# Kernel tuning notes

Measured on AMD Instinct MI355X. Metric: run time of the kernel, lower is better.

Reference implementation:

```python
import math
import jax, jax.numpy as jnp
import numpy as np

B, D, H = 8, 2048, 256

def setup_inputs() -> dict:
    key = jax.random.key(0)
    ks = jax.random.split(key, 8)
    s = 1.0 / math.sqrt(H)
    x = jax.random.normal(ks[0], (B, D, H), dtype=jnp.float32)
    adj = jax.random.randint(ks[1], (B, D, D), 0, 2, dtype=jnp.int32)
    Wq = jax.random.normal(ks[2], (H, H), dtype=jnp.float32) * s
    Wk = jax.random.normal(ks[3], (H, H), dtype=jnp.float32) * s
    Wv = jax.random.normal(ks[4], (H, H), dtype=jnp.float32) * s
    Wp = jax.random.normal(ks[5], (H, H), dtype=jnp.float32) * s
    bp = jax.random.normal(ks[6], (H,), dtype=jnp.float32) * 0.01
    gamma = jnp.ones((H,), dtype=jnp.float32)
    beta = jnp.zeros((H,), dtype=jnp.float32)
    return {"x": x, "adj": adj, "Wq": Wq, "Wk": Wk, "Wv": Wv,
            "Wp": Wp, "bp": bp, "gamma": gamma, "beta": beta}

def _layer_norm(h, gamma, beta, eps=1e-5):
    mu = jnp.mean(h, axis=-1, keepdims=True)
    var = jnp.mean(jnp.square(h - mu), axis=-1, keepdims=True)
    return (h - mu) * jax.lax.rsqrt(var + eps) * gamma + beta

def reference(x, adj, Wq, Wk, Wv, Wp, bp, gamma, beta):
    # torch Linear: y = x @ W.T
    q = jnp.einsum('bdh,oh->bdo', x, Wq)
    k = jnp.einsum('bdh,oh->bdo', x, Wk)
    v = jnp.einsum('bdh,oh->bdo', x, Wv)
    scores = jnp.einsum('bdo,beo->bde', q, k) / math.sqrt(H)
    scores = jnp.where(adj <= 0, jnp.float32(-1e9), scores)
    attn = jax.nn.softmax(scores, axis=-1)
    agg = jnp.einsum('bde,beo->bdo', attn, v)
    out = jnp.einsum('bdo,po->bdp', agg, Wp) + bp
    return _layer_norm(x + out, gamma, beta)
```

## Files before the change

kernel.cpp:

```cpp
#include <hip/hip_runtime.h>
#include <stdint.h>

#define NB 8
#define ND 2048
#define NH 256

typedef __attribute__((ext_vector_type(8))) short bf16x8;
typedef __attribute__((ext_vector_type(4))) float f32x4;
typedef __attribute__((ext_vector_type(16))) float f32x16;
typedef __attribute__((ext_vector_type(4))) int   i32x4;
typedef __attribute__((ext_vector_type(2))) unsigned int u32x2;
typedef __attribute__((ext_vector_type(4))) unsigned int u32x4;

#define MFMA16 __builtin_amdgcn_mfma_f32_16x16x32_bf16
#define MFMA32 __builtin_amdgcn_mfma_f32_32x32x16_bf16

__device__ __forceinline__ unsigned short f2bf(float f) {
    union { float f; unsigned int u; } c; c.f = f;
    unsigned int u = c.u + 0x7FFFu + ((c.u >> 16) & 1u);
    return (unsigned short)(u >> 16);
}
__device__ __forceinline__ unsigned int pack2(float a, float b) {
    return (unsigned int)f2bf(a) | ((unsigned int)f2bf(b) << 16);
}
__device__ __forceinline__ unsigned int cvtpk(float a, float b) {
    unsigned int r;
    asm("v_cvt_pk_bf16_f32 %0, %1, %2" : "=v"(r) : "v"(a), "v"(b));
    return r;
}
__device__ __forceinline__ void plswap(unsigned int& a, unsigned int& b) {
    asm volatile("v_permlane32_swap_b32 %0, %1" : "+v"(a), "+v"(b));
}
__device__ __forceinline__ bf16x8 mk8(unsigned int a, unsigned int b, unsigned int c, unsigned int d) {
    union { unsigned int u[4]; bf16x8 v; } x;
    x.u[0] = a; x.u[1] = b; x.u[2] = c; x.u[3] = d;
    return x.v;
}
__device__ __forceinline__ void gload_lds16(const void* g, void* l) {
    __builtin_amdgcn_global_load_lds(
        (const __attribute__((address_space(1))) void*)g,
        (__attribute__((address_space(3))) void*)l, 16, 0, 0);
}

__global__ __launch_bounds__(256) void qkv_kernel(
    const float* __restrict__ x,
    const float* __restrict__ Wq, const float* __restrict__ Wk, const float* __restrict__ Wv,
    unsigned short* __restrict__ qb, unsigned short* __restrict__ kb, unsigned short* __restrict__ vT)
{
    __shared__ unsigned short Wt[64][264];
    __shared__ unsigned short Xt[64][264];
    const int z  = blockIdx.z;
    const int m0 = blockIdx.x * 64;
    const int o0 = blockIdx.y * 64;
    const float* W = (z == 0) ? Wq : (z == 1 ? Wk : Wv);
    const int t = threadIdx.x;

#pragma unroll
    for (int i = 0; i < 16; ++i) {
        int fidx = i * 256 + t;
        int row = fidx >> 6, c4 = fidx & 63;
        f32x4 vW = *reinterpret_cast<const f32x4*>(W + (size_t)(o0 + row) * NH + c4 * 4);
        f32x4 vX = *reinterpret_cast<const f32x4*>(x + (size_t)(m0 + row) * NH + c4 * 4);
        u32x2 pw; pw[0] = pack2(vW[0], vW[1]); pw[1] = pack2(vW[2], vW[3]);
        u32x2 px; px[0] = pack2(vX[0], vX[1]); px[1] = pack2(vX[2], vX[3]);
        *reinterpret_cast<u32x2*>(&Wt[row][c4 * 4]) = pw;
        *reinterpret_cast<u32x2*>(&Xt[row][c4 * 4]) = px;
    }
    __syncthreads();

    const int w = t >> 6, lane = t & 63, lr = lane & 15, half = lane >> 4;
    const unsigned short (*Ab)[264] = (z == 2) ? Xt : Wt;
    const unsigned short (*Bb)[264] = (z == 2) ? Wt : Xt;
    const int ar0 = 32 * (w >> 1), br0 = 32 * (w & 1);

    f32x4 acc[2][2] = {};
#pragma unroll
    for (int kk = 0; kk < 8; ++kk) {
        bf16x8 a[2], bfr[2];
#pragma unroll
        for (int f = 0; f < 2; ++f) {
            a[f]   = *reinterpret_cast<const bf16x8*>(&Ab[ar0 + 16 * f + lr][32 * kk + 8 * half]);
            bfr[f] = *reinterpret_cast<const bf16x8*>(&Bb[br0 + 16 * f + lr][32 * kk + 8 * half]);
        }
#pragma unroll
        for (int fa = 0; fa < 2; ++fa)
#pragma unroll
            for (int fb = 0; fb < 2; ++fb)
                acc[fa][fb] = MFMA16(a[fa], bfr[fb], acc[fa][fb], 0, 0, 0);
    }

    if (z == 0) {
#pragma unroll
        for (int fa = 0; fa < 2; ++fa)
#pragma unroll
            for (int fb = 0; fb < 2; ++fb) {
                int m = m0 + br0 + 16 * fb + lr;
                int o = o0 + ar0 + 16 * fa + 4 * half;
                u32x2 pk; pk[0] = pack2(acc[fa][fb][0], acc[fa][fb][1]);
                pk[1] = pack2(acc[fa][fb][2], acc[fa][fb][3]);
                *reinterpret_cast<u32x2*>(qb + (size_t)m * NH + o) = pk;
            }
    } else if (z == 1) {
#pragma unroll
        for (int fa = 0; fa < 2; ++fa)
#pragma unroll
            for (int fb = 0; fb < 2; ++fb) {
                int m = m0 + br0 + 16 * fb + lr;
                int o = o0 + ar0 + 16 * fa + 4 * half;
                int bb = m >> 11, el = m & 2047;
                u32x2 pk; pk[0] = pack2(acc[fa][fb][0], acc[fa][fb][1]);
                pk[1] = pack2(acc[fa][fb][2], acc[fa][fb][3]);
                size_t idx = (((size_t)bb * 32 + (o >> 3)) * 2048 + el) * 8 + (o & 7);
                *reinterpret_cast<u32x2*>(kb + idx) = pk;
            }
    } else {
#pragma unroll
        for (int fa = 0; fa < 2; ++fa)
#pragma unroll
            for (int fb = 0; fb < 2; ++fb) {
                int dg = m0 + ar0 + 16 * fa + 4 * half;
                int o  = o0 + br0 + 16 * fb + lr;
                int bb = dg >> 11, el = dg & 2047;
                u32x2 pk; pk[0] = pack2(acc[fa][fb][0], acc[fa][fb][1]);
                pk[1] = pack2(acc[fa][fb][2], acc[fa][fb][3]);
                size_t idx = (((size_t)bb * 256 + (el >> 3)) * 256 + o) * 8 + (el & 7);
                *reinterpret_cast<u32x2*>(vT + idx) = pk;
            }
    }
}

template<int ESP, int SIDES>
__global__ __launch_bounds__(512, 2) void attn_kernel(
    const unsigned short* __restrict__ qb, const unsigned short* __restrict__ kb,
    const unsigned short* __restrict__ vT, const int* __restrict__ adj,
    unsigned short* __restrict__ part, float* __restrict__ mpart, float* __restrict__ lpart)
{
    constexpr int GROUPS = 8 / SIDES;
    constexpr int QB = 32 * GROUPS;
    constexpr int NOT = 8 / SIDES;
    constexpr int NT = (ND / ESP) / 32;
    constexpr int QTSH = (ESP == 4) ? 5 : 4;

    __shared__ unsigned char KT[2][16384];
    __shared__ unsigned char VTl[2][16384];

    const int bid = blockIdx.x;
    const int b = bid & 7, es = (bid >> 3) & (ESP - 1), qt = bid >> QTSH;
    const int t = threadIdx.x, w = t >> 6, l = t & 63;
    const int lo32 = l & 31, hi = l >> 5;
    const int g = w & (GROUPS - 1), side = w / GROUPS;
    const int qbase = qt * QB + g * 32;
    const int obase = side * (256 / SIDES);
    const int ebase = es * (ND / ESP);
    const float SC = 0.0625f, L2E = 1.44269504f;

    bf16x8 qf[16];
    {
        const unsigned short* qr = qb + ((size_t)b * ND + qbase + lo32) * NH + 8 * hi;
#pragma unroll
        for (int kk = 0; kk < 16; ++kk)
            qf[kk] = *reinterpret_cast<const bf16x8*>(qr + kk * 16);
    }

    const char* kbc = (const char*)kb + ((size_t)b << 20);
    const char* vtc = (const char*)vT + ((size_t)b << 20);
    const int* adjr = adj + ((size_t)b * ND + qbase + lo32) * ND + ebase;

    auto stageK = [&](int buf, int tt) {
        const int e0s = ebase + tt * 32;
#pragma unroll
        for (int i = 0; i < 2; ++i) {
            int off = i * 8192 + t * 16;
            int koct = off >> 9, e = (off >> 4) & 31;
            gload_lds16(kbc + (size_t)koct * 32768 + (size_t)(e0s + e) * 16, &KT[buf][off]);
        }
    };
    auto stageV = [&](int buf, int tt) {
        const int Eb = (ebase + tt * 32) >> 3;
#pragma unroll
        for (int i = 0; i < 2; ++i) {
            int off = i * 8192 + t * 16;
            int eoct = off >> 12, o = (off >> 4) & 255;
            gload_lds16(vtc + (size_t)(Eb + eoct) * 4096 + (size_t)o * 16, &VTl[buf][off]);
        }
    };

    f32x16 acc[NOT] = {};
    float m_run = -__builtin_inff(), l_run = 0.f;

    stageK(0, 0); stageV(0, 0);
    __syncthreads();

    for (int tt = 0; tt < NT; ++tt) {
        const int cur = tt & 1;
        if (tt < NT - 1) { stageK(cur ^ 1, tt + 1); stageV(cur ^ 1, tt + 1); }

        i32x4 aj[4];
#pragma unroll
        for (int gg = 0; gg < 4; ++gg)
            aj[gg] = *reinterpret_cast<const i32x4*>(adjr + tt * 32 + gg * 8 + 4 * hi);

        const char* Kc = (const char*)&KT[cur][0];
        f32x16 s = {};
#pragma unroll
        for (int kk = 0; kk < 16; ++kk) {
            bf16x8 kf = *reinterpret_cast<const bf16x8*>(Kc + kk * 1024 + hi * 512 + lo32 * 16);
            s = MFMA32(kf, qf[kk], s, 0, 0, 0);
        }

        float p[16];
        float tmax = -__builtin_inff();
#pragma unroll
        for (int gg = 0; gg < 4; ++gg)
#pragma unroll
            for (int r = 0; r < 4; ++r) {
                float sv = s[gg * 4 + r] * SC;
                sv = (aj[gg][r] > 0) ? sv : -1e9f;
                p[gg * 4 + r] = sv;
                tmax = fmaxf(tmax, sv);
            }
        tmax = fmaxf(tmax, __shfl_xor(tmax, 32));
        if (!__all(tmax <= m_run + 8.0f)) {
            const float m_new = fmaxf(m_run, tmax);
            const float scale = exp2f((m_run - m_new) * L2E);
#pragma unroll
            for (int ot = 0; ot < NOT; ++ot)
#pragma unroll
                for (int r = 0; r < 16; ++r) acc[ot][r] *= scale;
            l_run *= scale;
            m_run = m_new;
        }
        float psum = 0.f;
#pragma unroll
        for (int r2 = 0; r2 < 16; ++r2) {
            float pe = exp2f((p[r2] - m_run) * L2E);
            p[r2] = pe;
            psum += pe;
        }
        psum += __shfl_xor(psum, 32);
        l_run += psum;

        unsigned int c0 = cvtpk(p[0], p[1]),   c1 = cvtpk(p[2], p[3]);
        unsigned int c2 = cvtpk(p[4], p[5]),   c3 = cvtpk(p[6], p[7]);
        plswap(c0, c2); plswap(c1, c3);
        unsigned int c4 = cvtpk(p[8], p[9]),   c5 = cvtpk(p[10], p[11]);
        unsigned int c6 = cvtpk(p[12], p[13]), c7 = cvtpk(p[14], p[15]);
        plswap(c4, c6); plswap(c5, c7);
        const bf16x8 pf0 = mk8(c0, c1, c2, c3);
        const bf16x8 pf1 = mk8(c4, c5, c6, c7);

        const char* Vc = (const char*)&VTl[cur][0];
#pragma unroll
        for (int ot = 0; ot < NOT; ++ot) {
            bf16x8 vf = *reinterpret_cast<const bf16x8*>(
                Vc + hi * 4096 + (size_t)(obase + ot * 32 + lo32) * 16);
            acc[ot] = MFMA32(vf, pf0, acc[ot], 0, 0, 0);
        }
#pragma unroll
        for (int ot = 0; ot < NOT; ++ot) {
            bf16x8 vf = *reinterpret_cast<const bf16x8*>(
                Vc + 8192 + hi * 4096 + (size_t)(obase + ot * 32 + lo32) * 16);
            acc[ot] = MFMA32(vf, pf1, acc[ot], 0, 0, 0);
        }
        __syncthreads();
    }

    const int qg = b * ND + qbase + lo32;
    unsigned short* pb = part + ((size_t)es * 16384 + qg) * 256;
#pragma unroll
    for (int ot = 0; ot < NOT; ++ot)
#pragma unroll
        for (int g2 = 0; g2 < 4; ++g2) {
            u32x2 pk;
            pk[0] = pack2(acc[ot][g2 * 4 + 0], acc[ot][g2 * 4 + 1]);
            pk[1] = pack2(acc[ot][g2 * 4 + 2], acc[ot][g2 * 4 + 3]);
            *reinterpret_cast<u32x2*>(pb + obase + ot * 32 + g2 * 8 + 4 * hi) = pk;
        }
    if (hi == 0 && side == 0) {
        mpart[(size_t)es * 16384 + qg] = m_run;
        lpart[(size_t)es * 16384 + qg] = l_run;
    }
}

template<int ESP>
__global__ __launch_bounds__(256) void combine_kernel(
    const unsigned short* __restrict__ part, const float* __restrict__ mpart,
    const float* __restrict__ lpart, unsigned short* __restrict__ agg)
{
    const float L2E = 1.44269504f;
    const int t = threadIdx.x;
    const int row8 = t >> 5, cw = t & 31;
    const int q = blockIdx.x * 8 + row8;

    float me[ESP], le[ESP], M = -__builtin_inff();
#pragma unroll
    for (int e = 0; e < ESP; ++e) {
        me[e] = mpart[(size_t)e * 16384 + q];
        le[e] = lpart[(size_t)e * 16384 + q];
        M = fmaxf(M, me[e]);
    }
    float wsum = 0.f;
#pragma unroll
    for (int e = 0; e < ESP; ++e) { me[e] = exp2f((me[e] - M) * L2E); wsum += me[e] * le[e]; }
    const float inv = 1.f / wsum;

    float o[8] = {};
#pragma unroll
    for (int e = 0; e < ESP; ++e) {
        u32x4 v = *reinterpret_cast<const u32x4*>(part + ((size_t)e * 16384 + q) * 256 + cw * 8);
        const float ce = me[e] * inv;
#pragma unroll
        for (int j = 0; j < 4; ++j) {
            o[2 * j]     += ce * __uint_as_float(v[j] << 16);
            o[2 * j + 1] += ce * __uint_as_float(v[j] & 0xffff0000u);
        }
    }
    u32x4 pk;
#pragma unroll
    for (int j = 0; j < 4; ++j) pk[j] = pack2(o[2 * j], o[2 * j + 1]);
    *reinterpret_cast<u32x4*>(agg + (size_t)q * 256 + cw * 8) = pk;
}

__global__ __launch_bounds__(256) void oproj_kernel(
    const unsigned short* __restrict__ agg, const float* __restrict__ Wp,
    const float* __restrict__ bp, const float* __restrict__ x, float* __restrict__ h)
{
    __shared__ unsigned short Wt[64][264];
    __shared__ unsigned short Xt[64][264];
    const int m0 = blockIdx.x * 64, p0 = blockIdx.y * 64;
    const int t = threadIdx.x;

#pragma unroll
    for (int i = 0; i < 16; ++i) {
        int fidx = i * 256 + t, row = fidx >> 6, c4 = fidx & 63;
        f32x4 vW = *reinterpret_cast<const f32x4*>(Wp + (size_t)(p0 + row) * NH + c4 * 4);
        u32x2 pw; pw[0] = pack2(vW[0], vW[1]); pw[1] = pack2(vW[2], vW[3]);
        *reinterpret_cast<u32x2*>(&Wt[row][c4 * 4]) = pw;
    }
#pragma unroll
    for (int i = 0; i < 8; ++i) {
        int fidx = i * 256 + t, row = fidx >> 5, c8 = fidx & 31;
        u32x4 vA = *reinterpret_cast<const u32x4*>(agg + (size_t)(m0 + row) * NH + c8 * 8);
        *reinterpret_cast<u32x4*>(&Xt[row][c8 * 8]) = vA;
    }
    __syncthreads();

    const int w = t >> 6, lane = t & 63, lr = lane & 15, half = lane >> 4;
    const int ar0 = 32 * (w >> 1), br0 = 32 * (w & 1);

    f32x4 acc[2][2] = {};
#pragma unroll
    for (int kk = 0; kk < 8; ++kk) {
        bf16x8 a[2], bfr[2];
#pragma unroll
        for (int f = 0; f < 2; ++f) {
            a[f]   = *reinterpret_cast<const bf16x8*>(&Wt[ar0 + 16 * f + lr][32 * kk + 8 * half]);
            bfr[f] = *reinterpret_cast<const bf16x8*>(&Xt[br0 + 16 * f + lr][32 * kk + 8 * half]);
        }
#pragma unroll
        for (int fa = 0; fa < 2; ++fa)
#pragma unroll
            for (int fb = 0; fb < 2; ++fb)
                acc[fa][fb] = MFMA16(a[fa], bfr[fb], acc[fa][fb], 0, 0, 0);
    }

#pragma unroll
    for (int fa = 0; fa < 2; ++fa)
#pragma unroll
        for (int fb = 0; fb < 2; ++fb) {
            int pcol = p0 + ar0 + 16 * fa + 4 * half;
            int m = m0 + br0 + 16 * fb + lr;
            f32x4 bias = *reinterpret_cast<const f32x4*>(bp + pcol);
            f32x4 xr   = *reinterpret_cast<const f32x4*>(x + (size_t)m * NH + pcol);
            f32x4 out;
#pragma unroll
            for (int r = 0; r < 4; ++r) out[r] = acc[fa][fb][r] + bias[r] + xr[r];
            *reinterpret_cast<f32x4*>(h + (size_t)m * NH + pcol) = out;
        }
}

__global__ __launch_bounds__(256) void ln_kernel(
    const float* __restrict__ h, const float* __restrict__ gamma,
    const float* __restrict__ beta, float* __restrict__ out)
{
    const int t = threadIdx.x, w = t >> 6, lane = t & 63;
    const size_t row = (size_t)blockIdx.x * 4 + w;
    const float* hr = h + row * NH;
    f32x4 v = *reinterpret_cast<const f32x4*>(hr + lane * 4);
    float s = v[0] + v[1] + v[2] + v[3];
#pragma unroll
    for (int off = 1; off < 64; off <<= 1) s += __shfl_xor(s, off);
    const float mu = s * (1.f / 256.f);
    f32x4 dv; float q = 0.f;
#pragma unroll
    for (int r = 0; r < 4; ++r) { dv[r] = v[r] - mu; q += dv[r] * dv[r]; }
#pragma unroll
    for (int off = 1; off < 64; off <<= 1) q += __shfl_xor(q, off);
    const float rs = rsqrtf(q * (1.f / 256.f) + 1e-5f);
    f32x4 g  = *reinterpret_cast<const f32x4*>(gamma + lane * 4);
    f32x4 be = *reinterpret_cast<const f32x4*>(beta + lane * 4);
    f32x4 o;
#pragma unroll
    for (int r = 0; r < 4; ++r) o[r] = dv[r] * rs * g[r] + be[r];
    *reinterpret_cast<f32x4*>(out + row * NH + lane * 4) = o;
}

extern "C" void kernel_launch(void* const* d_in, const int* in_sizes, int n_in,
                              void* d_out, int out_size, void* d_ws, size_t ws_size,
                              hipStream_t stream)
{
    const float* x     = (const float*)d_in[0];
    const int*   adj   = (const int*)d_in[1];
    const float* Wq    = (const float*)d_in[2];
    const float* Wk    = (const float*)d_in[3];
    const float* Wv    = (const float*)d_in[4];
    const float* Wp    = (const float*)d_in[5];
    const float* bp    = (const float*)d_in[6];
    const float* gamma = (const float*)d_in[7];
    const float* beta  = (const float*)d_in[8];

    char* ws = (char*)d_ws;
    const size_t MB = 1024 * 1024;
    unsigned short* qb    = (unsigned short*)(ws);
    unsigned short* kb    = (unsigned short*)(ws + 8 * MB);
    unsigned short* vT    = (unsigned short*)(ws + 16 * MB);
    unsigned short* agg   = qb;
    unsigned short* partb = (unsigned short*)(ws + 24 * MB);
    float* h = (float*)(ws + 8 * MB);
    float* out = (float*)d_out;

    qkv_kernel<<<dim3(256, 4, 3), 256, 0, stream>>>(x, Wq, Wk, Wv, qb, kb, vT);

    const bool big = ws_size >= (size_t)57 * MB;
    if (big) {
        float* mpart = (float*)(ws + 56 * MB);
        float* lpart = (float*)(ws + 56 * MB + 256 * 1024);
        attn_kernel<4, 1><<<dim3(256), 512, 0, stream>>>(qb, kb, vT, adj, partb, mpart, lpart);
        combine_kernel<4><<<dim3(2048), 256, 0, stream>>>(partb, mpart, lpart, agg);
    } else {
        float* mpart = (float*)(ws + 40 * MB);
        float* lpart = (float*)(ws + 40 * MB + 128 * 1024);
        attn_kernel<2, 2><<<dim3(256), 512, 0, stream>>>(qb, kb, vT, adj, partb, mpart, lpart);
        combine_kernel<2><<<dim3(2048), 256, 0, stream>>>(partb, mpart, lpart, agg);
    }

    oproj_kernel<<<dim3(256, 4), 256, 0, stream>>>(agg, Wp, bp, x, h);
    ln_kernel<<<dim3(4096), 256, 0, stream>>>(h, gamma, beta, out);
}
```

Baseline: 122.5 us.

## Fuse combine, output projection and layernorm; widen attention key tiles; merge QKV blocks

The QKV projection now computes Q, K and V in one block, reusing the converted x tile and reloading only the weight tile. The attention kernel stages 64-key tiles instead of 32, processes them as two sub-steps, and raises wave priority around the MFMA sections. The split-softmax combine, output projection, bias/residual add and layernorm are merged into a single kernel that keeps rows in LDS, removing the intermediate fp32 h buffer and two launches. The trade-offs are much larger LDS per block, which may lower occupancy, and fewer, heavier blocks in the fused epilogue.

```diff
diff --git a/kernel.cpp b/kernel.cpp
--- a/kernel.cpp
+++ b/kernel.cpp
@@ -41,6 +41,8 @@
         (const __attribute__((address_space(1))) void*)g,
         (__attribute__((address_space(3))) void*)l, 16, 0, 0);
 }
+__device__ __forceinline__ float bflo(unsigned int u) { return __uint_as_float(u << 16); }
+__device__ __forceinline__ float bfhi(unsigned int u) { return __uint_as_float(u & 0xffff0000u); }
 
 __global__ __launch_bounds__(256) void qkv_kernel(
     const float* __restrict__ x,
@@ -49,17 +51,16 @@
 {
     __shared__ unsigned short Wt[64][264];
     __shared__ unsigned short Xt[64][264];
-    const int z  = blockIdx.z;
     const int m0 = blockIdx.x * 64;
     const int o0 = blockIdx.y * 64;
-    const float* W = (z == 0) ? Wq : (z == 1 ? Wk : Wv);
     const int t = threadIdx.x;
+    const int w = t >> 6, lane = t & 63, lr = lane & 15, half = lane >> 4;
+    const int ar0 = 32 * (w >> 1), br0 = 32 * (w & 1);
 
 #pragma unroll
     for (int i = 0; i < 16; ++i) {
-        int fidx = i * 256 + t;
-        int row = fidx >> 6, c4 = fidx & 63;
-        f32x4 vW = *reinterpret_cast<const f32x4*>(W + (size_t)(o0 + row) * NH + c4 * 4);
+        int fidx = i * 256 + t, row = fidx >> 6, c4 = fidx & 63;
+        f32x4 vW = *reinterpret_cast<const f32x4*>(Wq + (size_t)(o0 + row) * NH + c4 * 4);
         f32x4 vX = *reinterpret_cast<const f32x4*>(x + (size_t)(m0 + row) * NH + c4 * 4);
         u32x2 pw; pw[0] = pack2(vW[0], vW[1]); pw[1] = pack2(vW[2], vW[3]);
         u32x2 px; px[0] = pack2(vX[0], vX[1]); px[1] = pack2(vX[2], vX[3]);
@@ -68,64 +69,77 @@
     }
     __syncthreads();
 
-    const int w = t >> 6, lane = t & 63, lr = lane & 15, half = lane >> 4;
-    const unsigned short (*Ab)[264] = (z == 2) ? Xt : Wt;
-    const unsigned short (*Bb)[264] = (z == 2) ? Wt : Xt;
-    const int ar0 = 32 * (w >> 1), br0 = 32 * (w & 1);
-
-    f32x4 acc[2][2] = {};
-#pragma unroll
-    for (int kk = 0; kk < 8; ++kk) {
-        bf16x8 a[2], bfr[2];
-#pragma unroll
-        for (int f = 0; f < 2; ++f) {
-            a[f]   = *reinterpret_cast<const bf16x8*>(&Ab[ar0 + 16 * f + lr][32 * kk + 8 * half]);
-            bfr[f] = *reinterpret_cast<const bf16x8*>(&Bb[br0 + 16 * f + lr][32 * kk + 8 * half]);
-        }
-#pragma unroll
-        for (int fa = 0; fa < 2; ++fa)
-#pragma unroll
-            for (int fb = 0; fb < 2; ++fb)
-                acc[fa][fb] = MFMA16(a[fa], bfr[fb], acc[fa][fb], 0, 0, 0);
-    }
-
-    if (z == 0) {
-#pragma unroll
-        for (int fa = 0; fa < 2; ++fa)
-#pragma unroll
-            for (int fb = 0; fb < 2; ++fb) {
-                int m = m0 + br0 + 16 * fb + lr;
-                int o = o0 + ar0 + 16 * fa + 4 * half;
-                u32x2 pk; pk[0] = pack2(acc[fa][fb][0], acc[fa][fb][1]);
-                pk[1] = pack2(acc[fa][fb][2], acc[fa][fb][3]);
-                *reinterpret_cast<u32x2*>(qb + (size_t)m * NH + o) = pk;
-            }
-    } else if (z == 1) {
-#pragma unroll
-        for (int fa = 0; fa < 2; ++fa)
-#pragma unroll
-            for (int fb = 0; fb < 2; ++fb) {
-                int m = m0 + br0 + 16 * fb + lr;
-                int o = o0 + ar0 + 16 * fa + 4 * half;
-                int bb = m >> 11, el = m & 2047;
-                u32x2 pk; pk[0] = pack2(acc[fa][fb][0], acc[fa][fb][1]);
-                pk[1] = pack2(acc[fa][fb][2], acc[fa][fb][3]);
-                size_t idx = (((size_t)bb * 32 + (o >> 3)) * 2048 + el) * 8 + (o & 7);
-                *reinterpret_cast<u32x2*>(kb + idx) = pk;
-            }
-    } else {
-#pragma unroll
-        for (int fa = 0; fa < 2; ++fa)
-#pragma unroll
-            for (int fb = 0; fb < 2; ++fb) {
-                int dg = m0 + ar0 + 16 * fa + 4 * half;
-                int o  = o0 + br0 + 16 * fb + lr;
-                int bb = dg >> 11, el = dg & 2047;
-                u32x2 pk; pk[0] = pack2(acc[fa][fb][0], acc[fa][fb][1]);
-                pk[1] = pack2(acc[fa][fb][2], acc[fa][fb][3]);
-                size_t idx = (((size_t)bb * 256 + (el >> 3)) * 256 + o) * 8 + (el & 7);
-                *reinterpret_cast<u32x2*>(vT + idx) = pk;
-            }
+    for (int z = 0; z < 3; ++z) {
+        const unsigned short (*Ab)[264] = (z == 2) ? Xt : Wt;
+        const unsigned short (*Bb)[264] = (z == 2) ? Wt : Xt;
+
+        f32x4 acc[2][2] = {};
+#pragma unroll
+        for (int kk = 0; kk < 8; ++kk) {
+            bf16x8 a[2], bfr[2];
+#pragma unroll
+            for (int f = 0; f < 2; ++f) {
+                a[f]   = *reinterpret_cast<const bf16x8*>(&Ab[ar0 + 16 * f + lr][32 * kk + 8 * half]);
+                bfr[f] = *reinterpret_cast<const bf16x8*>(&Bb[br0 + 16 * f + lr][32 * kk + 8 * half]);
+            }
+#pragma unroll
+            for (int fa = 0; fa < 2; ++fa)
+#pragma unroll
+                for (int fb = 0; fb < 2; ++fb)
+                    acc[fa][fb] = MFMA16(a[fa], bfr[fb], acc[fa][fb], 0, 0, 0);
+        }
+
+        if (z == 0) {
+#pragma unroll
+            for (int fa = 0; fa < 2; ++fa)
+#pragma unroll
+                for (int fb = 0; fb < 2; ++fb) {
+                    int m = m0 + br0 + 16 * fb + lr;
+                    int o = o0 + ar0 + 16 * fa + 4 * half;
+                    u32x2 pk; pk[0] = pack2(acc[fa][fb][0], acc[fa][fb][1]);
+                    pk[1] = pack2(acc[fa][fb][2], acc[fa][fb][3]);
+                    *reinterpret_cast<u32x2*>(qb + (size_t)m * NH + o) = pk;
+                }
+        } else if (z == 1) {
+#pragma unroll
+            for (int fa = 0; fa < 2; ++fa)
+#pragma unroll
+                for (int fb = 0; fb < 2; ++fb) {
+                    int m = m0 + br0 + 16 * fb + lr;
+                    int o = o0 + ar0 + 16 * fa + 4 * half;
+                    int bb = m >> 11, el = m & 2047;
+                    u32x2 pk; pk[0] = pack2(acc[fa][fb][0], acc[fa][fb][1]);
+                    pk[1] = pack2(acc[fa][fb][2], acc[fa][fb][3]);
+                    size_t idx = (((size_t)bb * 32 + (o >> 3)) * 2048 + el) * 8 + (o & 7);
+                    *reinterpret_cast<u32x2*>(kb + idx) = pk;
+                }
+        } else {
+#pragma unroll
+            for (int fa = 0; fa < 2; ++fa)
+#pragma unroll
+                for (int fb = 0; fb < 2; ++fb) {
+                    int dg = m0 + ar0 + 16 * fa + 4 * half;
+                    int o  = o0 + br0 + 16 * fb + lr;
+                    int bb = dg >> 11, el = dg & 2047;
+                    u32x2 pk; pk[0] = pack2(acc[fa][fb][0], acc[fa][fb][1]);
+                    pk[1] = pack2(acc[fa][fb][2], acc[fa][fb][3]);
+                    size_t idx = (((size_t)bb * 256 + (el >> 3)) * 256 + o) * 8 + (el & 7);
+                    *reinterpret_cast<u32x2*>(vT + idx) = pk;
+                }
+        }
+
+        if (z < 2) {
+            __syncthreads();
+            const float* Wn = (z == 0) ? Wk : Wv;
+#pragma unroll
+            for (int i = 0; i < 16; ++i) {
+                int fidx = i * 256 + t, row = fidx >> 6, c4 = fidx & 63;
+                f32x4 vW = *reinterpret_cast<const f32x4*>(Wn + (size_t)(o0 + row) * NH + c4 * 4);
+                u32x2 pw; pw[0] = pack2(vW[0], vW[1]); pw[1] = pack2(vW[2], vW[3]);
+                *reinterpret_cast<u32x2*>(&Wt[row][c4 * 4]) = pw;
+            }
+            __syncthreads();
+        }
     }
 }
 
@@ -138,20 +152,20 @@
     constexpr int GROUPS = 8 / SIDES;
     constexpr int QB = 32 * GROUPS;
     constexpr int NOT = 8 / SIDES;
-    constexpr int NT = (ND / ESP) / 32;
+    constexpr int NT = (ND / ESP) / 64;
     constexpr int QTSH = (ESP == 4) ? 5 : 4;
 
-    __shared__ unsigned char KT[2][16384];
-    __shared__ unsigned char VTl[2][16384];
+    __shared__ unsigned char KT[2][32768];
+    __shared__ unsigned char VTl[2][32768];
 
     const int bid = blockIdx.x;
-    const int b = bid & 7, es = (bid >> 3) & (ESP - 1), qt = bid >> QTSH;
+    const int b = bid & 7, es0 = (bid >> 3) & (ESP - 1), qt = bid >> QTSH;
     const int t = threadIdx.x, w = t >> 6, l = t & 63;
     const int lo32 = l & 31, hi = l >> 5;
     const int g = w & (GROUPS - 1), side = w / GROUPS;
     const int qbase = qt * QB + g * 32;
     const int obase = side * (256 / SIDES);
-    const int ebase = es * (ND / ESP);
+    const int ebase = es0 * (ND / ESP);
     const float SC = 0.0625f, L2E = 1.44269504f;
 
     bf16x8 qf[16];
@@ -167,18 +181,18 @@
     const int* adjr = adj + ((size_t)b * ND + qbase + lo32) * ND + ebase;
 
     auto stageK = [&](int buf, int tt) {
-        const int e0s = ebase + tt * 32;
-#pragma unroll
-        for (int i = 0; i < 2; ++i) {
+        const int e0s = ebase + tt * 64;
+#pragma unroll
+        for (int i = 0; i < 4; ++i) {
             int off = i * 8192 + t * 16;
-            int koct = off >> 9, e = (off >> 4) & 31;
+            int koct = off >> 10, e = (off >> 4) & 63;
             gload_lds16(kbc + (size_t)koct * 32768 + (size_t)(e0s + e) * 16, &KT[buf][off]);
         }
     };
     auto stageV = [&](int buf, int tt) {
-        const int Eb = (ebase + tt * 32) >> 3;
-#pragma unroll
-        for (int i = 0; i < 2; ++i) {
+        const int Eb = (ebase + tt * 64) >> 3;
+#pragma unroll
+        for (int i = 0; i < 4; ++i) {
             int off = i * 8192 + t * 16;
             int eoct = off >> 12, o = (off >> 4) & 255;
             gload_lds16(vtc + (size_t)(Eb + eoct) * 4096 + (size_t)o * 16, &VTl[buf][off]);
@@ -195,78 +209,87 @@
         const int cur = tt & 1;
         if (tt < NT - 1) { stageK(cur ^ 1, tt + 1); stageV(cur ^ 1, tt + 1); }
 
-        i32x4 aj[4];
-#pragma unroll
-        for (int gg = 0; gg < 4; ++gg)
-            aj[gg] = *reinterpret_cast<const i32x4*>(adjr + tt * 32 + gg * 8 + 4 * hi);
-
         const char* Kc = (const char*)&KT[cur][0];
-        f32x16 s = {};
-#pragma unroll
-        for (int kk = 0; kk < 16; ++kk) {
-            bf16x8 kf = *reinterpret_cast<const bf16x8*>(Kc + kk * 1024 + hi * 512 + lo32 * 16);
-            s = MFMA32(kf, qf[kk], s, 0, 0, 0);
-        }
-
-        float p[16];
-        float tmax = -__builtin_inff();
-#pragma unroll
-        for (int gg = 0; gg < 4; ++gg)
-#pragma unroll
-            for (int r = 0; r < 4; ++r) {
-                float sv = s[gg * 4 + r] * SC;
-                sv = (aj[gg][r] > 0) ? sv : -1e9f;
-                p[gg * 4 + r] = sv;
-                tmax = fmaxf(tmax, sv);
-            }
-        tmax = fmaxf(tmax, __shfl_xor(tmax, 32));
-        if (!__all(tmax <= m_run + 8.0f)) {
-            const float m_new = fmaxf(m_run, tmax);
-            const float scale = exp2f((m_run - m_new) * L2E);
-#pragma unroll
-            for (int ot = 0; ot < NOT; ++ot)
-#pragma unroll
-                for (int r = 0; r < 16; ++r) acc[ot][r] *= scale;
-            l_run *= scale;
-            m_run = m_new;
-        }
-        float psum = 0.f;
-#pragma unroll
-        for (int r2 = 0; r2 < 16; ++r2) {
-            float pe = exp2f((p[r2] - m_run) * L2E);
-            p[r2] = pe;
-            psum += pe;
-        }
-        psum += __shfl_xor(psum, 32);
-        l_run += psum;
-
-        unsigned int c0 = cvtpk(p[0], p[1]),   c1 = cvtpk(p[2], p[3]);
-        unsigned int c2 = cvtpk(p[4], p[5]),   c3 = cvtpk(p[6], p[7]);
-        plswap(c0, c2); plswap(c1, c3);
-        unsigned int c4 = cvtpk(p[8], p[9]),   c5 = cvtpk(p[10], p[11]);
-        unsigned int c6 = cvtpk(p[12], p[13]), c7 = cvtpk(p[14], p[15]);
-        plswap(c4, c6); plswap(c5, c7);
-        const bf16x8 pf0 = mk8(c0, c1, c2, c3);
-        const bf16x8 pf1 = mk8(c4, c5, c6, c7);
-
         const char* Vc = (const char*)&VTl[cur][0];
-#pragma unroll
-        for (int ot = 0; ot < NOT; ++ot) {
-            bf16x8 vf = *reinterpret_cast<const bf16x8*>(
-                Vc + hi * 4096 + (size_t)(obase + ot * 32 + lo32) * 16);
-            acc[ot] = MFMA32(vf, pf0, acc[ot], 0, 0, 0);
-        }
-#pragma unroll
-        for (int ot = 0; ot < NOT; ++ot) {
-            bf16x8 vf = *reinterpret_cast<const bf16x8*>(
-                Vc + 8192 + hi * 4096 + (size_t)(obase + ot * 32 + lo32) * 16);
-            acc[ot] = MFMA32(vf, pf1, acc[ot], 0, 0, 0);
+
+#pragma unroll
+        for (int s = 0; s < 2; ++s) {
+            i32x4 aj[4];
+#pragma unroll
+            for (int gg = 0; gg < 4; ++gg)
+                aj[gg] = *reinterpret_cast<const i32x4*>(adjr + tt * 64 + s * 32 + gg * 8 + 4 * hi);
+
+            f32x16 sc = {};
+            __builtin_amdgcn_s_setprio(1);
+#pragma unroll
+            for (int kk = 0; kk < 16; ++kk) {
+                bf16x8 kf = *reinterpret_cast<const bf16x8*>(
+                    Kc + kk * 2048 + hi * 1024 + s * 512 + lo32 * 16);
+                sc = MFMA32(kf, qf[kk], sc, 0, 0, 0);
+            }
+            __builtin_amdgcn_s_setprio(0);
+
+            float p[16];
+            float tmax = -__builtin_inff();
+#pragma unroll
+            for (int gg = 0; gg < 4; ++gg)
+#pragma unroll
+                for (int r = 0; r < 4; ++r) {
+                    float sv = sc[gg * 4 + r] * SC;
+                    sv = (aj[gg][r] > 0) ? sv : -1e9f;
+                    p[gg * 4 + r] = sv;
+                    tmax = fmaxf(tmax, sv);
+                }
+            tmax = fmaxf(tmax, __shfl_xor(tmax, 32));
+            if (!__all(tmax <= m_run + 8.0f)) {
+                const float m_new = fmaxf(m_run, tmax);
+                const float scale = exp2f((m_run - m_new) * L2E);
+#pragma unroll
+                for (int ot = 0; ot < NOT; ++ot)
+#pragma unroll
+                    for (int r = 0; r < 16; ++r) acc[ot][r] *= scale;
+                l_run *= scale;
+                m_run = m_new;
+            }
+            float psum = 0.f;
+#pragma unroll
+            for (int r2 = 0; r2 < 16; ++r2) {
+                float pe = exp2f((p[r2] - m_run) * L2E);
+                p[r2] = pe;
+                psum += pe;
+            }
+            psum += __shfl_xor(psum, 32);
+            l_run += psum;
+
+            unsigned int c0 = cvtpk(p[0], p[1]),   c1 = cvtpk(p[2], p[3]);
+            unsigned int c2 = cvtpk(p[4], p[5]),   c3 = cvtpk(p[6], p[7]);
+            plswap(c0, c2); plswap(c1, c3);
+            unsigned int c4 = cvtpk(p[8], p[9]),   c5 = cvtpk(p[10], p[11]);
+            unsigned int c6 = cvtpk(p[12], p[13]), c7 = cvtpk(p[14], p[15]);
+            plswap(c4, c6); plswap(c5, c7);
+            const bf16x8 pf0 = mk8(c0, c1, c2, c3);
+            const bf16x8 pf1 = mk8(c4, c5, c6, c7);
+
+            __builtin_amdgcn_s_setprio(1);
+#pragma unroll
+            for (int ot = 0; ot < NOT; ++ot) {
+                bf16x8 vf = *reinterpret_cast<const bf16x8*>(
+                    Vc + s * 16384 + hi * 4096 + (size_t)(obase + ot * 32 + lo32) * 16);
+                acc[ot] = MFMA32(vf, pf0, acc[ot], 0, 0, 0);
+            }
+#pragma unroll
+            for (int ot = 0; ot < NOT; ++ot) {
+                bf16x8 vf = *reinterpret_cast<const bf16x8*>(
+                    Vc + s * 16384 + 8192 + hi * 4096 + (size_t)(obase + ot * 32 + lo32) * 16);
+                acc[ot] = MFMA32(vf, pf1, acc[ot], 0, 0, 0);
+            }
+            __builtin_amdgcn_s_setprio(0);
         }
         __syncthreads();
     }
 
     const int qg = b * ND + qbase + lo32;
-    unsigned short* pb = part + ((size_t)es * 16384 + qg) * 256;
+    unsigned short* pb = part + ((size_t)es0 * 16384 + qg) * 256;
 #pragma unroll
     for (int ot = 0; ot < NOT; ++ot)
 #pragma unroll
@@ -277,132 +300,140 @@
             *reinterpret_cast<u32x2*>(pb + obase + ot * 32 + g2 * 8 + 4 * hi) = pk;
         }
     if (hi == 0 && side == 0) {
-        mpart[(size_t)es * 16384 + qg] = m_run;
-        lpart[(size_t)es * 16384 + qg] = l_run;
+        mpart[(size_t)es0 * 16384 + qg] = m_run;
+        lpart[(size_t)es0 * 16384 + qg] = l_run;
     }
 }
 
 template<int ESP>
-__global__ __launch_bounds__(256) void combine_kernel(
+__global__ __launch_bounds__(256) void fuse_kernel(
     const unsigned short* __restrict__ part, const float* __restrict__ mpart,
-    const float* __restrict__ lpart, unsigned short* __restrict__ agg)
+    const float* __restrict__ lpart, const float* __restrict__ Wp,
+    const float* __restrict__ bp, const float* __restrict__ x,
+    const float* __restrict__ gamma, const float* __restrict__ beta,
+    float* __restrict__ out)
 {
+    __shared__ unsigned short Xt[64][264];
+    __shared__ unsigned short Wt[64][264];
+    __shared__ float hL[64][264];
+    __shared__ float cel[64][ESP];
+
+    const int M0 = blockIdx.x * 64;
+    const int t = threadIdx.x;
     const float L2E = 1.44269504f;
-    const int t = threadIdx.x;
-    const int row8 = t >> 5, cw = t & 31;
-    const int q = blockIdx.x * 8 + row8;
-
-    float me[ESP], le[ESP], M = -__builtin_inff();
-#pragma unroll
-    for (int e = 0; e < ESP; ++e) {
-        me[e] = mpart[(size_t)e * 16384 + q];
-        le[e] = lpart[(size_t)e * 16384 + q];
-        M = fmaxf(M, me[e]);
-    }
-    float wsum = 0.f;
-#pragma unroll
-    for (int e = 0; e < ESP; ++e) { me[e] = exp2f((me[e] - M) * L2E); wsum += me[e] * le[e]; }
-    const float inv = 1.f / wsum;
-
-    float o[8] = {};
-#pragma unroll
-    for (int e = 0; e < ESP; ++e) {
-        u32x4 v = *reinterpret_cast<const u32x4*>(part + ((size_t)e * 16384 + q) * 256 + cw * 8);
-        const float ce = me[e] * inv;
-#pragma unroll
-        for (int j = 0; j < 4; ++j) {
-            o[2 * j]     += ce * __uint_as_float(v[j] << 16);
-            o[2 * j + 1] += ce * __uint_as_float(v[j] & 0xffff0000u);
-        }
-    }
-    u32x4 pk;
-#pragma unroll
-    for (int j = 0; j < 4; ++j) pk[j] = pack2(o[2 * j], o[2 * j + 1]);
-    *reinterpret_cast<u32x4*>(agg + (size_t)q * 256 + cw * 8) = pk;
-}
-
-__global__ __launch_bounds__(256) void oproj_kernel(
-    const unsigned short* __restrict__ agg, const float* __restrict__ Wp,
-    const float* __restrict__ bp, const float* __restrict__ x, float* __restrict__ h)
-{
-    __shared__ unsigned short Wt[64][264];
-    __shared__ unsigned short Xt[64][264];
-    const int m0 = blockIdx.x * 64, p0 = blockIdx.y * 64;
-    const int t = threadIdx.x;
-
+
+    if (t < 64) {
+        float me[ESP], le[ESP], M = -__builtin_inff();
+#pragma unroll
+        for (int e = 0; e < ESP; ++e) {
+            me[e] = mpart[(size_t)e * 16384 + M0 + t];
+            le[e] = lpart[(size_t)e * 16384 + M0 + t];
+            M = fmaxf(M, me[e]);
+        }
+        float wsum = 0.f;
+#pragma unroll
+        for (int e = 0; e < ESP; ++e) { me[e] = exp2f((me[e] - M) * L2E); wsum += me[e] * le[e]; }
+        const float inv = 1.f / wsum;
+#pragma unroll
+        for (int e = 0; e < ESP; ++e) cel[t][e] = me[e] * inv;
+    }
 #pragma unroll
     for (int i = 0; i < 16; ++i) {
         int fidx = i * 256 + t, row = fidx >> 6, c4 = fidx & 63;
-        f32x4 vW = *reinterpret_cast<const f32x4*>(Wp + (size_t)(p0 + row) * NH + c4 * 4);
+        f32x4 vW = *reinterpret_cast<const f32x4*>(Wp + (size_t)row * NH + c4 * 4);
         u32x2 pw; pw[0] = pack2(vW[0], vW[1]); pw[1] = pack2(vW[2], vW[3]);
         *reinterpret_cast<u32x2*>(&Wt[row][c4 * 4]) = pw;
     }
+    __syncthreads();
+
 #pragma unroll
     for (int i = 0; i < 8; ++i) {
         int fidx = i * 256 + t, row = fidx >> 5, c8 = fidx & 31;
-        u32x4 vA = *reinterpret_cast<const u32x4*>(agg + (size_t)(m0 + row) * NH + c8 * 8);
-        *reinterpret_cast<u32x4*>(&Xt[row][c8 * 8]) = vA;
+        float o[8] = {};
+#pragma unroll
+        for (int e = 0; e < ESP; ++e) {
+            u32x4 v = *reinterpret_cast<const u32x4*>(
+                part + (((size_t)e * 16384 + M0 + row) * 256 + c8 * 8));
+            const float ce = cel[row][e];
+#pragma unroll
+            for (int j = 0; j < 4; ++j) {
+                o[2 * j]     += ce * bflo(v[j]);
+                o[2 * j + 1] += ce * bfhi(v[j]);
+            }
+        }
+        u32x4 pk;
+#pragma unroll
+        for (int j = 0; j < 4; ++j) pk[j] = pack2(o[2 * j], o[2 * j + 1]);
+        *reinterpret_cast<u32x4*>(&Xt[row][c8 * 8]) = pk;
     }
     __syncthreads();
 
     const int w = t >> 6, lane = t & 63, lr = lane & 15, half = lane >> 4;
     const int ar0 = 32 * (w >> 1), br0 = 32 * (w & 1);
 
-    f32x4 acc[2][2] = {};
-#pragma unroll
-    for (int kk = 0; kk < 8; ++kk) {
-        bf16x8 a[2], bfr[2];
-#pragma unroll
-        for (int f = 0; f < 2; ++f) {
-            a[f]   = *reinterpret_cast<const bf16x8*>(&Wt[ar0 + 16 * f + lr][32 * kk + 8 * half]);
-            bfr[f] = *reinterpret_cast<const bf16x8*>(&Xt[br0 + 16 * f + lr][32 * kk + 8 * half]);
+    for (int pc = 0; pc < 4; ++pc) {
+        f32x4 acc[2][2] = {};
+#pragma unroll
+        for (int kk = 0; kk < 8; ++kk) {
+            bf16x8 a[2], bfr[2];
+#pragma unroll
+            for (int f = 0; f < 2; ++f) {
+                a[f]   = *reinterpret_cast<const bf16x8*>(&Wt[ar0 + 16 * f + lr][32 * kk + 8 * half]);
+                bfr[f] = *reinterpret_cast<const bf16x8*>(&Xt[br0 + 16 * f + lr][32 * kk + 8 * half]);
+            }
+#pragma unroll
+            for (int fa = 0; fa < 2; ++fa)
+#pragma unroll
+                for (int fb = 0; fb < 2; ++fb)
+                    acc[fa][fb] = MFMA16(a[fa], bfr[fb], acc[fa][fb], 0, 0, 0);
         }
 #pragma unroll
         for (int fa = 0; fa < 2; ++fa)
 #pragma unroll
-            for (int fb = 0; fb < 2; ++fb)
-                acc[fa][fb] = MFMA16(a[fa], bfr[fb], acc[fa][fb], 0, 0, 0);
-    }
-
-#pragma unroll
-    for (int fa = 0; fa < 2; ++fa)
-#pragma unroll
-        for (int fb = 0; fb < 2; ++fb) {
-            int pcol = p0 + ar0 + 16 * fa + 4 * half;
-            int m = m0 + br0 + 16 * fb + lr;
-            f32x4 bias = *reinterpret_cast<const f32x4*>(bp + pcol);
-            f32x4 xr   = *reinterpret_cast<const f32x4*>(x + (size_t)m * NH + pcol);
-            f32x4 out;
-#pragma unroll
-            for (int r = 0; r < 4; ++r) out[r] = acc[fa][fb][r] + bias[r] + xr[r];
-            *reinterpret_cast<f32x4*>(h + (size_t)m * NH + pcol) = out;
-        }
-}
-
-__global__ __launch_bounds__(256) void ln_kernel(
-    const float* __restrict__ h, const float* __restrict__ gamma,
-    const float* __restrict__ beta, float* __restrict__ out)
-{
-    const int t = threadIdx.x, w = t >> 6, lane = t & 63;
-    const size_t row = (size_t)blockIdx.x * 4 + w;
-    const float* hr = h + row * NH;
-    f32x4 v = *reinterpret_cast<const f32x4*>(hr + lane * 4);
-    float s = v[0] + v[1] + v[2] + v[3];
-#pragma unroll
-    for (int off = 1; off < 64; off <<= 1) s += __shfl_xor(s, off);
-    const float mu = s * (1.f / 256.f);
-    f32x4 dv; float q = 0.f;
-#pragma unroll
-    for (int r = 0; r < 4; ++r) { dv[r] = v[r] - mu; q += dv[r] * dv[r]; }
-#pragma unroll
-    for (int off = 1; off < 64; off <<= 1) q += __shfl_xor(q, off);
-    const float rs = rsqrtf(q * (1.f / 256.f) + 1e-5f);
-    f32x4 g  = *reinterpret_cast<const f32x4*>(gamma + lane * 4);
+            for (int fb = 0; fb < 2; ++fb) {
+                int p = pc * 64 + ar0 + 16 * fa + 4 * half;
+                int m = br0 + 16 * fb + lr;
+                *reinterpret_cast<f32x4*>(&hL[m][p]) = acc[fa][fb];
+            }
+        if (pc < 3) {
+            __syncthreads();
+#pragma unroll
+            for (int i = 0; i < 16; ++i) {
+                int fidx = i * 256 + t, row = fidx >> 6, c4 = fidx & 63;
+                f32x4 vW = *reinterpret_cast<const f32x4*>(
+                    Wp + (size_t)((pc + 1) * 64 + row) * NH + c4 * 4);
+                u32x2 pw; pw[0] = pack2(vW[0], vW[1]); pw[1] = pack2(vW[2], vW[3]);
+                *reinterpret_cast<u32x2*>(&Wt[row][c4 * 4]) = pw;
+            }
+            __syncthreads();
+        }
+    }
+    __syncthreads();
+
+    f32x4 gm = *reinterpret_cast<const f32x4*>(gamma + lane * 4);
     f32x4 be = *reinterpret_cast<const f32x4*>(beta + lane * 4);
-    f32x4 o;
-#pragma unroll
-    for (int r = 0; r < 4; ++r) o[r] = dv[r] * rs * g[r] + be[r];
-    *reinterpret_cast<f32x4*>(out + row * NH + lane * 4) = o;
+    f32x4 bv = *reinterpret_cast<const f32x4*>(bp + lane * 4);
+    for (int rr = 0; rr < 16; ++rr) {
+        const int row = w * 16 + rr;
+        f32x4 v = *reinterpret_cast<const f32x4*>(&hL[row][lane * 4]);
+        f32x4 xr = *reinterpret_cast<const f32x4*>(x + (size_t)(M0 + row) * NH + lane * 4);
+#pragma unroll
+        for (int r = 0; r < 4; ++r) v[r] += xr[r] + bv[r];
+        float s = v[0] + v[1] + v[2] + v[3];
+#pragma unroll
+        for (int off = 1; off < 64; off <<= 1) s += __shfl_xor(s, off);
+        const float mu = s * (1.f / 256.f);
+        f32x4 dv; float q = 0.f;
+#pragma unroll
+        for (int r = 0; r < 4; ++r) { dv[r] = v[r] - mu; q += dv[r] * dv[r]; }
+#pragma unroll
+        for (int off = 1; off < 64; off <<= 1) q += __shfl_xor(q, off);
+        const float rs = rsqrtf(q * (1.f / 256.f) + 1e-5f);
+        f32x4 o;
+#pragma unroll
+        for (int r = 0; r < 4; ++r) o[r] = dv[r] * rs * gm[r] + be[r];
+        *reinterpret_cast<f32x4*>(out + (size_t)(M0 + row) * NH + lane * 4) = o;
+    }
 }
 
 extern "C" void kernel_launch(void* const* d_in, const int* in_sizes, int n_in,
@@ -424,26 +455,21 @@
     unsigned short* qb    = (unsigned short*)(ws);
     unsigned short* kb    = (unsigned short*)(ws + 8 * MB);
     unsigned short* vT    = (unsigned short*)(ws + 16 * MB);
-    unsigned short* agg   = qb;
     unsigned short* partb = (unsigned short*)(ws + 24 * MB);
-    float* h = (float*)(ws + 8 * MB);
     float* out = (float*)d_out;
 
-    qkv_kernel<<<dim3(256, 4, 3), 256, 0, stream>>>(x, Wq, Wk, Wv, qb, kb, vT);
+    qkv_kernel<<<dim3(256, 4), 256, 0, stream>>>(x, Wq, Wk, Wv, qb, kb, vT);
 
     const bool big = ws_size >= (size_t)57 * MB;
     if (big) {
         float* mpart = (float*)(ws + 56 * MB);
         float* lpart = (float*)(ws + 56 * MB + 256 * 1024);
         attn_kernel<4, 1><<<dim3(256), 512, 0, stream>>>(qb, kb, vT, adj, partb, mpart, lpart);
-        combine_kernel<4><<<dim3(2048), 256, 0, stream>>>(partb, mpart, lpart, agg);
+        fuse_kernel<4><<<dim3(256), 256, 0, stream>>>(partb, mpart, lpart, Wp, bp, x, gamma, beta, out);
     } else {
         float* mpart = (float*)(ws + 40 * MB);
         float* lpart = (float*)(ws + 40 * MB + 128 * 1024);
         attn_kernel<2, 2><<<dim3(256), 512, 0, stream>>>(qb, kb, vT, adj, partb, mpart, lpart);
-        combine_kernel<2><<<dim3(2048), 256, 0, stream>>>(partb, mpart, lpart, agg);
-    }
-
-    oproj_kernel<<<dim3(256, 4), 256, 0, stream>>>(agg, Wp, bp, x, h);
-    ln_kernel<<<dim3(4096), 256, 0, stream>>>(h, gamma, beta, out);
-}
+        fuse_kernel<2><<<dim3(256), 256, 0, stream>>>(partb, mpart, lpart, Wp, bp, x, gamma, beta, out);
+    }
+}
```

After: 118.5 us. -3.2%, faster.
